# Optimization experiments

Measured on AMD Instinct MI355X. Metric: run time of the kernel, lower is better.

The kernel has to match this reference:

```python
import jax, jax.numpy as jnp
import numpy as np

B, T, C = 4, 2048, 1024
H = 16
HS = C // H          # 64
FF = 4 * C           # 4096
EPS = 1e-5


def layernorm(x, g, b):
    mu = jnp.mean(x, axis=-1, keepdims=True)
    var = jnp.mean(jnp.square(x - mu), axis=-1, keepdims=True)
    return (x - mu) * jax.lax.rsqrt(var + EPS) * g + b


def setup_inputs() -> dict:
    key = jax.random.key(0)
    ks = jax.random.split(key, 16)
    s_in = 1.0 / np.sqrt(C)
    s_ff = 1.0 / np.sqrt(FF)
    return {
        "x": jax.random.normal(ks[0], (B, T, C), jnp.float32),
        # per-head Q/K/V projections stacked: [H, C, HS]
        "Wq": jax.random.normal(ks[1], (H, C, HS), jnp.float32) * s_in,
        "Wk": jax.random.normal(ks[2], (H, C, HS), jnp.float32) * s_in,
        "Wv": jax.random.normal(ks[3], (H, C, HS), jnp.float32) * s_in,
        "Wproj": jax.random.normal(ks[4], (C, C), jnp.float32) * s_in,
        "bproj": jnp.zeros((C,), jnp.float32),
        "W1": jax.random.normal(ks[5], (C, FF), jnp.float32) * s_in,
        "b1": jnp.zeros((FF,), jnp.float32),
        "W2": jax.random.normal(ks[6], (FF, C), jnp.float32) * s_ff,
        "b2": jnp.zeros((C,), jnp.float32),
        "ln1_g": jnp.ones((C,), jnp.float32),
        "ln1_b": jnp.zeros((C,), jnp.float32),
        "ln2_g": jnp.ones((C,), jnp.float32),
        "ln2_b": jnp.zeros((C,), jnp.float32),
    }


def reference(x, Wq, Wk, Wv, Wproj, bproj, W1, b1, W2, b2,
              ln1_g, ln1_b, ln2_g, ln2_b):
    # --- multi-head causal self-attention on layernorm1(x) ---
    h = layernorm(x, ln1_g, ln1_b)                       # [B,T,C]
    q = jnp.einsum('btc,hcd->bhtd', h, Wq)
    k = jnp.einsum('btc,hcd->bhtd', h, Wk)
    v = jnp.einsum('btc,hcd->bhtd', h, Wv)
    scores = jnp.einsum('bhtd,bhsd->bhts', q, k) * (HS ** -0.5)
    causal = jnp.tril(jnp.ones((T, T), bool))
    scores = jnp.where(causal, scores, -jnp.inf)
    att = jax.nn.softmax(scores, axis=-1)                # [B,H,T,T]
    o = jnp.einsum('bhts,bhsd->bthd', att, v).reshape(B, T, C)  # head concat
    x = x + o @ Wproj + bproj
    # --- feedforward on layernorm2(x) ---
    h2 = layernorm(x, ln2_g, ln2_b)
    ff = jax.nn.relu(h2 @ W1 + b1) @ W2 + b2
    return x + ff
```

## Files before the change

kernel.cpp:

```cpp
#include <hip/hip_runtime.h>
#include <cstddef>
#include <cstdio>

#define Bn   4
#define Tn   2048
#define Cn   1024
#define Hn   16
#define HSn  64
#define FFn  4096
#define ROWS (Bn*Tn)
#define QKVW (3*Cn)

typedef __attribute__((ext_vector_type(8))) __bf16 bf16x8;
typedef __attribute__((ext_vector_type(4))) float f32x4;

__device__ __forceinline__ unsigned short f2bf(float f){
  unsigned int u = __float_as_uint(f);
  unsigned int r = (u + 0x7fffu + ((u >> 16) & 1u)) >> 16;
  return (unsigned short)r;
}

#define GLD16(g, l) __builtin_amdgcn_global_load_lds( \
    (__attribute__((address_space(1))) void*)(void*)(g), \
    (__attribute__((address_space(3))) void*)(l), 16, 0, 0)

__device__ __forceinline__ float wave_sum_f(float v){
#pragma unroll
  for (int o = 32; o > 0; o >>= 1) v += __shfl_xor(v, o);
  return v;
}

__global__ void ln_bf16(const float* __restrict__ x, const float* __restrict__ g,
                        const float* __restrict__ bb, unsigned short* __restrict__ y){
  const int row = blockIdx.x;
  const int tid = threadIdx.x;
  const float4 v = reinterpret_cast<const float4*>(x + (size_t)row * Cn)[tid];
  float s  = v.x + v.y + v.z + v.w;
  float ss = v.x*v.x + v.y*v.y + v.z*v.z + v.w*v.w;
  s = wave_sum_f(s); ss = wave_sum_f(ss);
  __shared__ float sm[4], sm2[4];
  const int w = tid >> 6, lane = tid & 63;
  if (lane == 0){ sm[w] = s; sm2[w] = ss; }
  __syncthreads();
  const float tot  = sm[0] + sm[1] + sm[2] + sm[3];
  const float tot2 = sm2[0] + sm2[1] + sm2[2] + sm2[3];
  const float mu = tot * (1.0f / Cn);
  const float rs = rsqrtf(tot2 * (1.0f / Cn) - mu * mu + 1e-5f);
  const float4 gv = reinterpret_cast<const float4*>(g)[tid];
  const float4 bv = reinterpret_cast<const float4*>(bb)[tid];
  ushort4 o;
  o.x = f2bf((v.x - mu) * rs * gv.x + bv.x);
  o.y = f2bf((v.y - mu) * rs * gv.y + bv.y);
  o.z = f2bf((v.z - mu) * rs * gv.z + bv.z);
  o.w = f2bf((v.w - mu) * rs * gv.w + bv.w);
  reinterpret_cast<ushort4*>(y + (size_t)row * Cn)[tid] = o;
}

__global__ void transpose_cast(const float* __restrict__ in, unsigned short* __restrict__ out,
                               int R, int Cc){
  __shared__ float t[64][65];
  const int tid = threadIdx.x;
  const int r0 = blockIdx.y * 64, c0 = blockIdx.x * 64;
  const int rb = tid >> 6, cl = tid & 63;
#pragma unroll
  for (int j = 0; j < 16; ++j)
    t[rb + j*4][cl] = in[(size_t)(r0 + rb + j*4) * Cc + c0 + cl];
  __syncthreads();
#pragma unroll
  for (int j = 0; j < 16; ++j)
    out[(size_t)(c0 + rb + j*4) * R + r0 + cl] = f2bf(t[cl][rb + j*4]);
}

__global__ void repack_qkv_t(const float* __restrict__ Wq, const float* __restrict__ Wk,
                             const float* __restrict__ Wv, unsigned short* __restrict__ Wrt){
  __shared__ float t[64][65];
  const int tid = threadIdx.x;
  const int kb = blockIdx.x * 64;
  const int hh = blockIdx.y;
  const int sec = hh >> 4, h = hh & 15;
  const float* W = (sec == 0) ? Wq : ((sec == 1) ? Wk : Wv);
  const int rb = tid >> 6, dl = tid & 63;
#pragma unroll
  for (int j = 0; j < 16; ++j)
    t[rb + j*4][dl] = W[h * (Cn*HSn) + (size_t)(kb + rb + j*4) * HSn + dl];
  __syncthreads();
#pragma unroll
  for (int j = 0; j < 16; ++j)
    Wrt[(size_t)(sec*Cn + h*64 + rb + j*4) * Cn + kb + dl] = f2bf(t[dl][rb + j*4]);
}

template<int RELU, int OUT_BF16>
__global__ __launch_bounds__(512, 2)
void gemm256(const unsigned short* __restrict__ A, const unsigned short* __restrict__ Bt,
             void* __restrict__ Cout, int M, int N, int K,
             const float* __restrict__ bias, const float* __restrict__ resid){
  __shared__ __align__(16) unsigned short As[4 * 8192];
  __shared__ __align__(16) unsigned short Bs[4 * 8192];
  const int tid  = threadIdx.x;
  const int wid  = tid >> 6, lane = tid & 63;
  const int wm   = wid >> 2, wn = wid & 3;
  const int fr   = lane & 15, Lq = lane >> 4;

  const int id  = blockIdx.x + gridDim.x * blockIdx.y;
  const int Nbn = gridDim.x;
  const int cpx = (gridDim.x * gridDim.y) >> 3;
  const int wg  = (id & 7) * cpx + (id >> 3);
  const int bm  = wg / Nbn;
  const int bn  = wg - bm * Nbn;

  const int srow  = wid * 8 + (lane >> 3);
  const int skoff = (((lane & 7) ^ (srow & 7)) * 8);
  const unsigned short* Abase = A  + (size_t)(bm * 256 + srow) * K + skoff;
  const unsigned short* Bbase = Bt + (size_t)(bn * 256 + srow) * K + skoff;

  auto stA = [&](int t, int h){
    const unsigned short* g0 = Abase + (size_t)h * 128 * K + (size_t)t * 64;
    unsigned short* l0 = As + (((2*t + h) & 3) * 8192) + wid * 512;
    GLD16(g0, l0);
    GLD16(g0 + (size_t)64 * K, l0 + 4096);
  };
  auto stB = [&](int t, int h){
    const unsigned short* g0 = Bbase + (size_t)h * 128 * K + (size_t)t * 64;
    unsigned short* l0 = Bs + (((2*t + h) & 3) * 8192) + wid * 512;
    GLD16(g0, l0);
    GLD16(g0 + (size_t)64 * K, l0 + 4096);
  };

  f32x4 acc[8][4] = {};
  const int NT = K >> 6;

  stA(0, 0); stA(0, 1); stB(0, 0); stB(0, 1);

  for (int t = 0; t < NT; ++t){
    const unsigned short* aS = As + (((2*t + wm) & 3) * 8192);
    const unsigned short* bS = Bs + (((2*t + (wn >> 1)) & 3) * 8192)
                                  + ((wn & 1) * 64) * 64;
    const bool pf = (t + 1 < NT);

    if (pf){ stA(t+1, 0); stA(t+1, 1); stB(t+1, 0); stB(t+1, 1); }
    __builtin_amdgcn_sched_barrier(0);
    if (pf) asm volatile("s_waitcnt vmcnt(8)");
    else    asm volatile("s_waitcnt vmcnt(0)");
    __builtin_amdgcn_s_barrier();

#pragma unroll
    for (int kk = 0; kk < 2; ++kk){
      const int kx = (((kk*4) + Lq) ^ (fr & 7)) * 8;
      bf16x8 bfv[4], af[4];
#pragma unroll
      for (int ni = 0; ni < 4; ++ni)
        bfv[ni] = *reinterpret_cast<const bf16x8*>(&bS[(ni*16 + fr) * 64 + kx]);
#pragma unroll
      for (int m2 = 0; m2 < 4; ++m2)
        af[m2] = *reinterpret_cast<const bf16x8*>(&aS[(m2*16 + fr) * 64 + kx]);
#pragma unroll
      for (int m2 = 0; m2 < 4; ++m2)
#pragma unroll
        for (int ni = 0; ni < 4; ++ni)
          acc[m2][ni] = __builtin_amdgcn_mfma_f32_16x16x32_bf16(
              af[m2], bfv[ni], acc[m2][ni], 0, 0, 0);
#pragma unroll
      for (int m2 = 0; m2 < 4; ++m2)
        af[m2] = *reinterpret_cast<const bf16x8*>(&aS[((4+m2)*16 + fr) * 64 + kx]);
#pragma unroll
      for (int m2 = 0; m2 < 4; ++m2)
#pragma unroll
        for (int ni = 0; ni < 4; ++ni)
          acc[4+m2][ni] = __builtin_amdgcn_mfma_f32_16x16x32_bf16(
              af[m2], bfv[ni], acc[4+m2][ni], 0, 0, 0);
    }
    __builtin_amdgcn_sched_barrier(0);
    __builtin_amdgcn_s_barrier();
  }

  const int lc = fr, lr4 = Lq * 4;
#pragma unroll
  for (int ni = 0; ni < 4; ++ni){
    const int col = bn*256 + wn*64 + ni*16 + lc;
    const float bv = bias ? bias[col] : 0.f;
#pragma unroll
    for (int mi = 0; mi < 8; ++mi){
      const int rowb = bm*256 + wm*128 + mi*16 + lr4;
#pragma unroll
      for (int r = 0; r < 4; ++r){
        float v = acc[mi][ni][r] + bv;
        if (RELU) v = fmaxf(v, 0.f);
        if (resid) v += resid[(size_t)(rowb + r) * N + col];
        if (OUT_BF16)
          ((unsigned short*)Cout)[(size_t)(rowb + r) * N + col] = f2bf(v);
        else
          ((float*)Cout)[(size_t)(rowb + r) * N + col] = v;
      }
    }
  }
}

template<int RELU, int OUT_BF16>
__global__ __launch_bounds__(256, 2)
void gemm128ring(const unsigned short* __restrict__ A, const unsigned short* __restrict__ Bt,
                 void* __restrict__ Cout, int M, int N, int K,
                 const float* __restrict__ bias, const float* __restrict__ resid){
  __shared__ __align__(16) unsigned short As[2 * 8192];
  __shared__ __align__(16) unsigned short Bs[2 * 8192];
  const int tid  = threadIdx.x;
  const int wave = tid >> 6, lane = tid & 63;
  const int wm   = wave >> 1, wn = wave & 1;
  const int fr   = lane & 15, Lq = lane >> 4;

  const int id  = blockIdx.x + gridDim.x * blockIdx.y;
  const int Nbn = gridDim.x;
  const int cpx = (gridDim.x * gridDim.y) >> 3;
  const int wg  = (id & 7) * cpx + (id >> 3);
  const int bm  = wg / Nbn;
  const int bn  = wg - bm * Nbn;

  const int srow  = tid >> 3;
  const int skoff = (((tid & 7) ^ (srow & 7)) * 8);
  const unsigned short* Abase = A  + (size_t)(bm * 128 + srow) * K + skoff;
  const unsigned short* Bbase = Bt + (size_t)(bn * 128 + srow) * K + skoff;

  auto stA = [&](int t){
    const unsigned short* g0 = Abase + (size_t)t * 64;
    unsigned short* l0 = As + ((t & 1) * 8192) + tid * 8;
#pragma unroll
    for (int j = 0; j < 4; ++j)
      GLD16(g0 + (size_t)(j*32) * K, l0 + j*2048);
  };
  auto stB = [&](int t){
    const unsigned short* g0 = Bbase + (size_t)t * 64;
    unsigned short* l0 = Bs + ((t & 1) * 8192) + tid * 8;
#pragma unroll
    for (int j = 0; j < 4; ++j)
      GLD16(g0 + (size_t)(j*32) * K, l0 + j*2048);
  };

  f32x4 acc[4][4] = {};
  const int NT = K >> 6;

  stA(0); stB(0);

  for (int t = 0; t < NT; ++t){
    const unsigned short* aS = As + ((t & 1) * 8192);
    const unsigned short* bS = Bs + ((t & 1) * 8192);
    const bool pf = (t + 1 < NT);

    if (pf){ stA(t+1); stB(t+1); }
    __builtin_amdgcn_sched_barrier(0);
    if (pf) asm volatile("s_waitcnt vmcnt(8)");
    else    asm volatile("s_waitcnt vmcnt(0)");
    __builtin_amdgcn_s_barrier();

#pragma unroll
    for (int kk = 0; kk < 2; ++kk){
      const int kx = (((kk*4) + Lq) ^ (fr & 7)) * 8;
      bf16x8 bfv[4], af[4];
#pragma unroll
      for (int ni = 0; ni < 4; ++ni)
        bfv[ni] = *reinterpret_cast<const bf16x8*>(&bS[(wn*64 + ni*16 + fr) * 64 + kx]);
#pragma unroll
      for (int mi = 0; mi < 4; ++mi)
        af[mi] = *reinterpret_cast<const bf16x8*>(&aS[(wm*64 + mi*16 + fr) * 64 + kx]);
#pragma unroll
      for (int mi = 0; mi < 4; ++mi)
#pragma unroll
        for (int ni = 0; ni < 4; ++ni)
          acc[mi][ni] = __builtin_amdgcn_mfma_f32_16x16x32_bf16(
              af[mi], bfv[ni], acc[mi][ni], 0, 0, 0);
    }
    __builtin_amdgcn_sched_barrier(0);
    __builtin_amdgcn_s_barrier();
  }

  const int lc = fr, lr4 = Lq * 4;
#pragma unroll
  for (int ni = 0; ni < 4; ++ni){
    const int col = bn*128 + wn*64 + ni*16 + lc;
    const float bv = bias ? bias[col] : 0.f;
#pragma unroll
    for (int mi = 0; mi < 4; ++mi){
      const int rowb = bm*128 + wm*64 + mi*16 + lr4;
#pragma unroll
      for (int r = 0; r < 4; ++r){
        float v = acc[mi][ni][r] + bv;
        if (RELU) v = fmaxf(v, 0.f);
        if (resid) v += resid[(size_t)(rowb + r) * N + col];
        if (OUT_BF16)
          ((unsigned short*)Cout)[(size_t)(rowb + r) * N + col] = f2bf(v);
        else
          ((float*)Cout)[(size_t)(rowb + r) * N + col] = v;
      }
    }
  }
}

__global__ void blockify_kv(const unsigned short* __restrict__ qkv,
                            unsigned short* __restrict__ Kb,
                            unsigned short* __restrict__ Vb){
  const int st = blockIdx.x, h = blockIdx.y, b = blockIdx.z;
  const int tid = threadIdx.x;
  const size_t base = ((size_t)(b*Hn + h)*32 + st) * 4096;
#pragma unroll
  for (int it = 0; it < 2; ++it){
    const int idx = it*256 + tid;
    const int s = idx >> 3, d8 = idx & 7;
    const uint4 v = *reinterpret_cast<const uint4*>(
        qkv + (size_t)(b*Tn + st*64 + s)*QKVW + Cn + h*64 + d8*8);
    *reinterpret_cast<uint4*>(Kb + base + d8*512 + ((s ^ d8) * 8)) = v;
  }
#pragma unroll
  for (int it = 0; it < 2; ++it){
    const int idx = it*256 + tid;
    const int d = idx & 63, s8 = idx >> 6;
    unsigned short tmp[8];
#pragma unroll
    for (int j = 0; j < 8; ++j)
      tmp[j] = qkv[(size_t)(b*Tn + st*64 + s8*8 + j)*QKVW + 2*Cn + h*64 + d];
    ushort4 lo, hi;
    lo.x = tmp[0]; lo.y = tmp[1]; lo.z = tmp[2]; lo.w = tmp[3];
    hi.x = tmp[4]; hi.y = tmp[5]; hi.z = tmp[6]; hi.w = tmp[7];
    *reinterpret_cast<ushort4*>(Vb + base + s8*512 + ((d ^ s8) * 8))     = lo;
    *reinterpret_cast<ushort4*>(Vb + base + s8*512 + ((d ^ s8) * 8) + 4) = hi;
  }
}

__global__ __launch_bounds__(512, 2)
void attn_mfma3(const unsigned short* __restrict__ qkv,
                const unsigned short* __restrict__ Kb,
                const unsigned short* __restrict__ Vb,
                unsigned short* __restrict__ O){
  __shared__ __align__(16) unsigned short Kls[2][4096];
  __shared__ __align__(16) unsigned short Vls[2][4096];
  __shared__ __align__(16) unsigned short Pt[8][16][72];

  const int bh = blockIdx.x;
  const int b = bh >> 4, h = bh & 15;
  const int pg = blockIdx.y;
  const int tid = threadIdx.x;
  const int wv = tid >> 6, l = tid & 63;
  const int strip = (wv < 4) ? pg : (7 - pg);
  const int qblk = strip*4 + (wv & 3);
  const int Lq = l >> 4, fr = l & 15;
  const int maxst = (7 - pg)*4 + 3;

  const size_t kvbase = ((size_t)(b*Hn + h) * 32) * 4096;

  union U { uint4 u; bf16x8 v; };
  U qf[4][2];
  const unsigned short* Qbase = qkv + ((size_t)(b*Tn + qblk*64)) * QKVW + h*64;
#pragma unroll
  for (int f = 0; f < 4; ++f){
    const unsigned short* qr = Qbase + (size_t)(f*16 + fr) * QKVW + Lq*8;
    qf[f][0].u = *reinterpret_cast<const uint4*>(qr);
    qf[f][1].u = *reinterpret_cast<const uint4*>(qr + 32);
  }

  f32x4 Oa[4][4] = {};
  float lsum[4] = {0.f, 0.f, 0.f, 0.f};
  const float C1 = 0.18033688011112042f;
  const float C2 = 28.853900817779268f;

  auto stage = [&](int st, int buf){
    const unsigned short* gk = Kb + kvbase + (size_t)st*4096 + wv*512 + l*8;
    const unsigned short* gv = Vb + kvbase + (size_t)st*4096 + wv*512 + l*8;
    GLD16(gk, &Kls[buf][wv*512]);
    GLD16(gv, &Vls[buf][wv*512]);
  };

  stage(0, 0);

  for (int st = 0; st <= maxst; ++st){
    const int buf = st & 1;
    __syncthreads();
    if (st < maxst) stage(st + 1, buf ^ 1);
    if (st > qblk) continue;

    U k0[4], k1[4];
#pragma unroll
    for (int sb = 0; sb < 4; ++sb){
      const int s = sb*16 + fr;
      k0[sb].u = *reinterpret_cast<const uint4*>(&Kls[buf][ Lq   *512 + ((s ^  Lq   ) * 8)]);
      k1[sb].u = *reinterpret_cast<const uint4*>(&Kls[buf][(4+Lq)*512 + ((s ^ (4+Lq)) * 8)]);
    }
    U v0[4], v1[4];
#pragma unroll
    for (int db = 0; db < 4; ++db){
      const int d = db*16 + fr;
      v0[db].u = *reinterpret_cast<const uint4*>(&Vls[buf][ Lq   *512 + ((d ^  Lq   ) * 8)]);
      v1[db].u = *reinterpret_cast<const uint4*>(&Vls[buf][(4+Lq)*512 + ((d ^ (4+Lq)) * 8)]);
    }

    const bool diag = (st == qblk);
#pragma unroll
    for (int f = 0; f < 4; ++f){
      f32x4 S[4];
#pragma unroll
      for (int sb = 0; sb < 4; ++sb){
        f32x4 z = {0.f, 0.f, 0.f, 0.f};
        z     = __builtin_amdgcn_mfma_f32_16x16x32_bf16(k0[sb].v, qf[f][0].v, z, 0, 0, 0);
        S[sb] = __builtin_amdgcn_mfma_f32_16x16x32_bf16(k1[sb].v, qf[f][1].v, z, 0, 0, 0);
      }
#pragma unroll
      for (int sb = 0; sb < 4; ++sb){
        float p0 = exp2f(fmaf(S[sb][0], C1, -C2));
        float p1 = exp2f(fmaf(S[sb][1], C1, -C2));
        float p2 = exp2f(fmaf(S[sb][2], C1, -C2));
        float p3 = exp2f(fmaf(S[sb][3], C1, -C2));
        if (diag){
          const int s0 = sb*16 + Lq*4, q = f*16 + fr;
          if (s0 + 0 > q) p0 = 0.f;
          if (s0 + 1 > q) p1 = 0.f;
          if (s0 + 2 > q) p2 = 0.f;
          if (s0 + 3 > q) p3 = 0.f;
        }
        lsum[f] += (p0 + p1) + (p2 + p3);
        const unsigned int pk0 = (unsigned int)f2bf(p0) | ((unsigned int)f2bf(p1) << 16);
        const unsigned int pk1 = (unsigned int)f2bf(p2) | ((unsigned int)f2bf(p3) << 16);
        *reinterpret_cast<uint2*>(&Pt[wv][fr][sb*16 + Lq*4]) = make_uint2(pk0, pk1);
      }
      U pf0, pf1;
      pf0.u = *reinterpret_cast<const uint4*>(&Pt[wv][fr][Lq*8]);
      pf1.u = *reinterpret_cast<const uint4*>(&Pt[wv][fr][32 + Lq*8]);
#pragma unroll
      for (int db = 0; db < 4; ++db){
        Oa[db][f] = __builtin_amdgcn_mfma_f32_16x16x32_bf16(v0[db].v, pf0.v, Oa[db][f], 0, 0, 0);
        Oa[db][f] = __builtin_amdgcn_mfma_f32_16x16x32_bf16(v1[db].v, pf1.v, Oa[db][f], 0, 0, 0);
      }
    }
  }

#pragma unroll
  for (int f = 0; f < 4; ++f){
    float s = lsum[f];
    s += __shfl_xor(s, 16);
    s += __shfl_xor(s, 32);
    const float inv = 1.0f / s;
    const size_t orow = (size_t)(b*Tn + qblk*64 + f*16 + fr);
#pragma unroll
    for (int db = 0; db < 4; ++db){
      ushort4 o;
      o.x = f2bf(Oa[db][f][0] * inv);
      o.y = f2bf(Oa[db][f][1] * inv);
      o.z = f2bf(Oa[db][f][2] * inv);
      o.w = f2bf(Oa[db][f][3] * inv);
      *reinterpret_cast<ushort4*>(&O[orow*Cn + h*64 + db*16 + Lq*4]) = o;
    }
  }
}

extern "C" void kernel_launch(void* const* d_in, const int* in_sizes, int n_in,
                              void* d_out, int out_size, void* d_ws, size_t ws_size,
                              hipStream_t stream){
  const float* x     = (const float*)d_in[0];
  const float* Wq    = (const float*)d_in[1];
  const float* Wk    = (const float*)d_in[2];
  const float* Wv    = (const float*)d_in[3];
  const float* Wproj = (const float*)d_in[4];
  const float* bproj = (const float*)d_in[5];
  const float* W1    = (const float*)d_in[6];
  const float* b1    = (const float*)d_in[7];
  const float* W2    = (const float*)d_in[8];
  const float* b2    = (const float*)d_in[9];
  const float* ln1_g = (const float*)d_in[10];
  const float* ln1_b = (const float*)d_in[11];
  const float* ln2_g = (const float*)d_in[12];
  const float* ln2_b = (const float*)d_in[13];
  float* out = (float*)d_out;

  const size_t MB = 1024ull * 1024ull;
  if (ws_size < 192ull * MB){
    fprintf(stderr, "kernel_launch: need 192MB workspace, got %zu\n", ws_size);
    return;
  }
  char* ws = (char*)d_ws;
  float*          x1    = (float*)(ws + 0);
  unsigned short* h     = (unsigned short*)(ws + 32 * MB);
  unsigned short* qkvb  = (unsigned short*)(ws + 48 * MB);
  unsigned short* ff1   = (unsigned short*)(ws + 48 * MB);
  unsigned short* Kb    = (unsigned short*)(ws + 96 * MB);
  unsigned short* Vb    = (unsigned short*)(ws + 112 * MB);
  unsigned short* Ob    = (unsigned short*)(ws + 128 * MB);
  unsigned short* Wrt   = (unsigned short*)(ws + 144 * MB);
  unsigned short* Wpt   = (unsigned short*)(ws + 150 * MB);
  unsigned short* W1t   = (unsigned short*)(ws + 152 * MB);
  unsigned short* W2t   = (unsigned short*)(ws + 160 * MB);

  repack_qkv_t<<<dim3(Cn/64, 3*Hn), 256, 0, stream>>>(Wq, Wk, Wv, Wrt);
  transpose_cast<<<dim3(Cn/64,  Cn/64),  256, 0, stream>>>(Wproj, Wpt, Cn,  Cn);
  transpose_cast<<<dim3(FFn/64, Cn/64),  256, 0, stream>>>(W1,    W1t, Cn,  FFn);
  transpose_cast<<<dim3(Cn/64,  FFn/64), 256, 0, stream>>>(W2,    W2t, FFn, Cn);

  ln_bf16<<<ROWS, 256, 0, stream>>>(x, ln1_g, ln1_b, h);
  gemm256<0,1><<<dim3(QKVW/256, ROWS/256), 512, 0, stream>>>(
      h, Wrt, qkvb, ROWS, QKVW, Cn, nullptr, nullptr);
  blockify_kv<<<dim3(Tn/64, Hn, Bn), 256, 0, stream>>>(qkvb, Kb, Vb);
  attn_mfma3<<<dim3(64, 4), 512, 0, stream>>>(qkvb, Kb, Vb, Ob);
  gemm128ring<0,0><<<dim3(Cn/128, ROWS/128), 256, 0, stream>>>(
      Ob, Wpt, x1, ROWS, Cn, Cn, bproj, x);
  ln_bf16<<<ROWS, 256, 0, stream>>>(x1, ln2_g, ln2_b, h);
  gemm256<1,1><<<dim3(FFn/256, ROWS/256), 512, 0, stream>>>(
      h, W1t, ff1, ROWS, FFn, Cn, b1, nullptr);
  gemm128ring<0,0><<<dim3(Cn/128, ROWS/128), 256, 0, stream>>>(
      ff1, W2t, out, ROWS, Cn, FFn, b2, x1);
}
```

Measured before the change: 546.9 us.

## Read K/V tiles directly from global memory and shrink attention blocks to four waves

Drops the LDS double-buffered K/V staging and its per-tile block barriers. Each wave now loads its swizzled K/V fragments straight from global memory (relying on L2/L1 for reuse) and loops only up to its own causal bound. Blocks shrink to 256 threads with 8 query groups per head, each wave taking a balanced pair of strips. This removes barrier stalls and idle waves on the diagonal, at the cost of redundant global/L2 traffic and no explicit prefetch.

After: 585.7 us. +7.1%, slower.

```diff
diff --git a/kernel.cpp b/kernel.cpp
--- a/kernel.cpp
+++ b/kernel.cpp
@@ -323,24 +323,21 @@
   }
 }
 
-__global__ __launch_bounds__(512, 2)
-void attn_mfma3(const unsigned short* __restrict__ qkv,
+__global__ __launch_bounds__(256, 2)
+void attn_mfma4(const unsigned short* __restrict__ qkv,
                 const unsigned short* __restrict__ Kb,
                 const unsigned short* __restrict__ Vb,
                 unsigned short* __restrict__ O){
-  __shared__ __align__(16) unsigned short Kls[2][4096];
-  __shared__ __align__(16) unsigned short Vls[2][4096];
-  __shared__ __align__(16) unsigned short Pt[8][16][72];
+  __shared__ __align__(16) unsigned short Pt[4][16][72];
 
   const int bh = blockIdx.x;
   const int b = bh >> 4, h = bh & 15;
-  const int pg = blockIdx.y;
+  const int qg = blockIdx.y;
   const int tid = threadIdx.x;
   const int wv = tid >> 6, l = tid & 63;
-  const int strip = (wv < 4) ? pg : (7 - pg);
-  const int qblk = strip*4 + (wv & 3);
+  const int qblk = (wv == 0) ? qg : (wv == 1) ? (qg + 8)
+                 : (wv == 2) ? (23 - qg) : (31 - qg);
   const int Lq = l >> 4, fr = l & 15;
-  const int maxst = (7 - pg)*4 + 3;
 
   const size_t kvbase = ((size_t)(b*Hn + h) * 32) * 4096;
 
@@ -359,34 +356,23 @@
   const float C1 = 0.18033688011112042f;
   const float C2 = 28.853900817779268f;
 
-  auto stage = [&](int st, int buf){
-    const unsigned short* gk = Kb + kvbase + (size_t)st*4096 + wv*512 + l*8;
-    const unsigned short* gv = Vb + kvbase + (size_t)st*4096 + wv*512 + l*8;
-    GLD16(gk, &Kls[buf][wv*512]);
-    GLD16(gv, &Vls[buf][wv*512]);
-  };
-
-  stage(0, 0);
-
-  for (int st = 0; st <= maxst; ++st){
-    const int buf = st & 1;
-    __syncthreads();
-    if (st < maxst) stage(st + 1, buf ^ 1);
-    if (st > qblk) continue;
+  for (int st = 0; st <= qblk; ++st){
+    const unsigned short* Kt = Kb + kvbase + (size_t)st * 4096;
+    const unsigned short* Vt = Vb + kvbase + (size_t)st * 4096;
 
     U k0[4], k1[4];
 #pragma unroll
     for (int sb = 0; sb < 4; ++sb){
       const int s = sb*16 + fr;
-      k0[sb].u = *reinterpret_cast<const uint4*>(&Kls[buf][ Lq   *512 + ((s ^  Lq   ) * 8)]);
-      k1[sb].u = *reinterpret_cast<const uint4*>(&Kls[buf][(4+Lq)*512 + ((s ^ (4+Lq)) * 8)]);
+      k0[sb].u = *reinterpret_cast<const uint4*>(&Kt[ Lq   *512 + ((s ^  Lq   ) * 8)]);
+      k1[sb].u = *reinterpret_cast<const uint4*>(&Kt[(4+Lq)*512 + ((s ^ (4+Lq)) * 8)]);
     }
     U v0[4], v1[4];
 #pragma unroll
     for (int db = 0; db < 4; ++db){
       const int d = db*16 + fr;
-      v0[db].u = *reinterpret_cast<const uint4*>(&Vls[buf][ Lq   *512 + ((d ^  Lq   ) * 8)]);
-      v1[db].u = *reinterpret_cast<const uint4*>(&Vls[buf][(4+Lq)*512 + ((d ^ (4+Lq)) * 8)]);
+      v0[db].u = *reinterpret_cast<const uint4*>(&Vt[ Lq   *512 + ((d ^  Lq   ) * 8)]);
+      v1[db].u = *reinterpret_cast<const uint4*>(&Vt[(4+Lq)*512 + ((d ^ (4+Lq)) * 8)]);
     }
 
     const bool diag = (st == qblk);
@@ -493,7 +479,7 @@
   gemm256<0,1><<<dim3(QKVW/256, ROWS/256), 512, 0, stream>>>(
       h, Wrt, qkvb, ROWS, QKVW, Cn, nullptr, nullptr);
   blockify_kv<<<dim3(Tn/64, Hn, Bn), 256, 0, stream>>>(qkvb, Kb, Vb);
-  attn_mfma3<<<dim3(64, 4), 512, 0, stream>>>(qkvb, Kb, Vb, Ob);
+  attn_mfma4<<<dim3(64, 8), 256, 0, stream>>>(qkvb, Kb, Vb, Ob);
   gemm128ring<0,0><<<dim3(Cn/128, ROWS/128), 256, 0, stream>>>(
       Ob, Wpt, x1, ROWS, Cn, Cn, bproj, x);
   ln_bf16<<<ROWS, 256, 0, stream>>>(x1, ln2_g, ln2_b, h);
```
